# Performance work log

Hardware: AMD Instinct MI355X
Metric: run time of the kernel (lower is better)

## Reference

```python
import jax, jax.numpy as jnp
import numpy as np

HIDDEN = 100
N_NODE = 100000
B = 512
T = 50

def setup_inputs() -> dict:
    key = jax.random.key(0)
    ks = jax.random.split(key, 20)
    stdv = 1.0 / np.sqrt(HIDDEN)
    u = lambda k, shape: jax.random.uniform(k, shape, jnp.float32, -stdv, stdv)
    d = HIDDEN
    return {
        "adj_in": jax.random.uniform(ks[0], (B, T, T), jnp.float32),
        "adj_out": jax.random.uniform(ks[1], (B, T, T), jnp.float32),
        "mask": jnp.ones((B, T), jnp.float32),
        "item": jax.random.randint(ks[2], (B, T), 0, N_NODE, jnp.int32),
        "alias": jax.random.randint(ks[3], (B, T), 0, T, jnp.int32),
        "step": 1,
        "embedding": u(ks[4], (N_NODE, d)),
        "W_in": u(ks[5], (d, d)),
        "b_in": u(ks[6], (d,)),
        "W_out": u(ks[7], (d, d)),
        "b_out": u(ks[8], (d,)),
        "gru_gate_k": u(ks[9], (3 * d, 2 * d)),
        "gru_gate_b": jnp.ones((2 * d,), jnp.float32),  # TF GRUCell gate bias init = 1.0
        "gru_cand_k": u(ks[10], (3 * d, d)),
        "gru_cand_b": jnp.zeros((d,), jnp.float32),
        "nasr_w1": u(ks[11], (d, d)),
        "nasr_w2": u(ks[12], (d, d)),
        "nasr_v": u(ks[13], (1, d)),
        "nasr_b": jnp.zeros((d,), jnp.float32),
        "B_mat": u(ks[14], (2 * d, d)),
    }


def _ggnn(item, adj_in, adj_out, embedding, W_in, b_in, W_out, b_out,
          gru_gate_k, gru_gate_b, gru_cand_k, gru_cand_b, step):
    h = embedding[item]  # [B,T,d]
    d = h.shape[-1]
    for _ in range(step):
        a_in = jnp.einsum('bts,bsd->btd', adj_in, h @ W_in + b_in)
        a_out = jnp.einsum('bts,bsd->btd', adj_out, h @ W_out + b_out)
        a = jnp.concatenate([a_in, a_out], axis=-1)  # [B,T,2d]
        # TF GRUCell: gates then candidate
        gates = jax.nn.sigmoid(jnp.concatenate([a, h], -1) @ gru_gate_k + gru_gate_b)
        r, u_ = gates[..., :d], gates[..., d:]
        c = jnp.tanh(jnp.concatenate([a, r * h], -1) @ gru_cand_k + gru_cand_b)
        h = u_ * h + (1.0 - u_) * c
    return h  # [B,T,d]


def reference(adj_in, adj_out, mask, item, alias, step, embedding,
              W_in, b_in, W_out, b_out, gru_gate_k, gru_gate_b,
              gru_cand_k, gru_cand_b, nasr_w1, nasr_w2, nasr_v, nasr_b, B_mat):
    d = embedding.shape[1]
    re_emb = _ggnn(item, adj_in, adj_out, embedding, W_in, b_in, W_out, b_out,
                   gru_gate_k, gru_gate_b, gru_cand_k, gru_cand_b, step)
    rm = jnp.sum(jax.lax.stop_gradient(mask), axis=1)  # session lengths
    bidx = jnp.arange(re_emb.shape[0])
    last_id = alias[bidx, rm.astype(jnp.int32) - 1]          # [B]
    last_h = re_emb[bidx, last_id]                            # [B,d]
    seq_h = jnp.take_along_axis(re_emb, alias[..., None], axis=1)  # [B,L,d]
    last = last_h @ nasr_w1                                   # [B,d]
    seq = seq_h @ nasr_w2                                     # [B,L,d]
    m = jax.nn.sigmoid(last[:, None, :] + seq + nasr_b)       # [B,L,d]
    coef = (m @ nasr_v[0]) * mask                             # [B,L]
    ma = jnp.concatenate([jnp.sum(coef[..., None] * seq_h, axis=1), last], axis=-1)  # [B,2d]
    y1 = ma @ B_mat                                           # [B,d]
    logits = y1 @ embedding[1:].T                             # [B,n_node-1]
    return logits
```

## Files before the change

### kernel.cpp

```cpp
#include <hip/hip_runtime.h>
#include <math.h>

#define D 100
#define T 50
#define BB 512
#define NOUT 99999

__device__ __forceinline__ float sigf(float x) { return 1.f / (1.f + expf(-x)); }

__global__ __launch_bounds__(256) void ggnn_fused(
    const float* __restrict__ adj_in, const float* __restrict__ adj_out,
    const float* __restrict__ mask,   const int* __restrict__ item,
    const int* __restrict__ alias_,   const float* __restrict__ emb,
    const float* __restrict__ W_in,   const float* __restrict__ b_in,
    const float* __restrict__ W_out,  const float* __restrict__ b_out,
    const float* __restrict__ gate_k, const float* __restrict__ gate_b,
    const float* __restrict__ cand_k, const float* __restrict__ cand_b,
    const float* __restrict__ w1,     const float* __restrict__ w2,
    const float* __restrict__ v,      const float* __restrict__ nb,
    const float* __restrict__ Bm,     float* __restrict__ y1)
{
    __shared__ float hS[T*D];
    __shared__ float R1[T*D];
    __shared__ float R2[T*D];
    __shared__ float maskS[T+2], vS[D], nbS[D], lastWS[D], coefS[T+2], maS[2*D];
    __shared__ int aliasS[T+2];
    __shared__ int rmidx;

    const int b = blockIdx.x, tid = threadIdx.x;
    const size_t bT = (size_t)b * T;

    if (tid < T) {
        aliasS[tid] = alias_[bT + tid];
        maskS[tid]  = mask[bT + tid];
    }
    if (tid >= 64 && tid < 64 + D) {
        int k = tid - 64;
        vS[k] = v[k]; nbS[k] = nb[k];
    }
    for (int idx = tid; idx < T*25; idx += 256) {
        int t = idx / 25, q = idx - t*25;
        int node = item[bT + t];
        *(float4*)&hS[t*D + q*4] = *(const float4*)&emb[(size_t)node*D + q*4];
    }
    __syncthreads();
    if (tid == 0) {
        float s = 0.f;
        for (int t = 0; t < T; ++t) s += maskS[t];
        rmidx = aliasS[(int)s - 1];
    }

    const bool act250 = tid < 250;
    const int tg50  = tid / 50;
    const int rem50 = tid % 50;
    const int cg25  = tid / 25;
    const int jq25  = tid % 25;

    if (act250) {
        const int which = rem50 / 25, jq = rem50 % 25;
        const int t0 = tg50 * 10;
        const float* W  = which ? W_out : W_in;
        const float* bb = which ? b_out : b_in;
        float4 binit = *(const float4*)&bb[jq*4];
        float4 acc[10];
        #pragma unroll
        for (int tt = 0; tt < 10; ++tt) acc[tt] = binit;
        for (int k = 0; k < D; k += 2) {
            float4 wa = *(const float4*)&W[k*D + jq*4];
            float4 wb = *(const float4*)&W[(k+1)*D + jq*4];
            #pragma unroll
            for (int tt = 0; tt < 10; ++tt) {
                float2 a = *(const float2*)&hS[(t0+tt)*D + k];
                acc[tt].x += a.x*wa.x + a.y*wb.x;
                acc[tt].y += a.x*wa.y + a.y*wb.y;
                acc[tt].z += a.x*wa.z + a.y*wb.z;
                acc[tt].w += a.x*wa.w + a.y*wb.w;
            }
        }
        float* dst = which ? R2 : R1;
        #pragma unroll
        for (int tt = 0; tt < 10; ++tt)
            *(float4*)&dst[(t0+tt)*D + jq*4] = acc[tt];
    }
    __syncthreads();

    float4 eacc[10];
    if (act250) {
        const int which = rem50 / 25, jq = rem50 % 25;
        const int t0 = tg50 * 10;
        const float* adj = which ? adj_out : adj_in;
        const float* Xs  = which ? R2 : R1;
        #pragma unroll
        for (int tt = 0; tt < 10; ++tt) eacc[tt] = make_float4(0.f,0.f,0.f,0.f);
        #pragma unroll 2
        for (int s = 0; s < T; ++s) {
            float4 x = *(const float4*)&Xs[s*D + jq*4];
            const float* ap = &adj[(bT + t0)*T + s];
            #pragma unroll
            for (int tt = 0; tt < 10; ++tt) {
                float a = ap[tt*T];
                eacc[tt].x += a*x.x; eacc[tt].y += a*x.y;
                eacc[tt].z += a*x.z; eacc[tt].w += a*x.w;
            }
        }
    }
    __syncthreads();
    if (act250) {
        const int which = rem50 / 25, jq = rem50 % 25;
        const int t0 = tg50 * 10;
        float* dst = which ? R2 : R1;
        #pragma unroll
        for (int tt = 0; tt < 10; ++tt)
            *(float4*)&dst[(t0+tt)*D + jq*4] = eacc[tt];
    }
    __syncthreads();

    float4 gacc[10];
    if (act250) {
        const int nq = rem50;
        const int t0 = tg50 * 10;
        float4 ginit = *(const float4*)&gate_b[nq*4];
        #pragma unroll
        for (int tt = 0; tt < 10; ++tt) gacc[tt] = ginit;
        for (int k = 0; k < D; k += 2) {
            float4 g0a = *(const float4*)&gate_k[(size_t)k*200 + nq*4];
            float4 g0b = *(const float4*)&gate_k[(size_t)(k+1)*200 + nq*4];
            float4 g1a = *(const float4*)&gate_k[(size_t)(k+100)*200 + nq*4];
            float4 g1b = *(const float4*)&gate_k[(size_t)(k+101)*200 + nq*4];
            float4 g2a = *(const float4*)&gate_k[(size_t)(k+200)*200 + nq*4];
            float4 g2b = *(const float4*)&gate_k[(size_t)(k+201)*200 + nq*4];
            #pragma unroll
            for (int tt = 0; tt < 10; ++tt) {
                float2 a0 = *(const float2*)&R1[(t0+tt)*D + k];
                float2 a1 = *(const float2*)&R2[(t0+tt)*D + k];
                float2 a2 = *(const float2*)&hS[(t0+tt)*D + k];
                gacc[tt].x += a0.x*g0a.x + a0.y*g0b.x + a1.x*g1a.x + a1.y*g1b.x + a2.x*g2a.x + a2.y*g2b.x;
                gacc[tt].y += a0.x*g0a.y + a0.y*g0b.y + a1.x*g1a.y + a1.y*g1b.y + a2.x*g2a.y + a2.y*g2b.y;
                gacc[tt].z += a0.x*g0a.z + a0.y*g0b.z + a1.x*g1a.z + a1.y*g1b.z + a2.x*g2a.z + a2.y*g2b.z;
                gacc[tt].w += a0.x*g0a.w + a0.y*g0b.w + a1.x*g1a.w + a1.y*g1b.w + a2.x*g2a.w + a2.y*g2b.w;
            }
        }
        #pragma unroll
        for (int tt = 0; tt < 10; ++tt) {
            gacc[tt].x = sigf(gacc[tt].x); gacc[tt].y = sigf(gacc[tt].y);
            gacc[tt].z = sigf(gacc[tt].z); gacc[tt].w = sigf(gacc[tt].w);
        }
    }

    float4 cacc[5];
    if (act250) {
        const int t0 = cg25 * 5;
        float4 cinit = *(const float4*)&cand_b[jq25*4];
        #pragma unroll
        for (int tt = 0; tt < 5; ++tt) cacc[tt] = cinit;
        for (int k = 0; k < D; k += 2) {
            float4 c0a = *(const float4*)&cand_k[(size_t)k*D + jq25*4];
            float4 c0b = *(const float4*)&cand_k[(size_t)(k+1)*D + jq25*4];
            float4 c1a = *(const float4*)&cand_k[(size_t)(k+100)*D + jq25*4];
            float4 c1b = *(const float4*)&cand_k[(size_t)(k+101)*D + jq25*4];
            #pragma unroll
            for (int tt = 0; tt < 5; ++tt) {
                float2 a0 = *(const float2*)&R1[(t0+tt)*D + k];
                float2 a1 = *(const float2*)&R2[(t0+tt)*D + k];
                cacc[tt].x += a0.x*c0a.x + a0.y*c0b.x + a1.x*c1a.x + a1.y*c1b.x;
                cacc[tt].y += a0.x*c0a.y + a0.y*c0b.y + a1.x*c1a.y + a1.y*c1b.y;
                cacc[tt].z += a0.x*c0a.z + a0.y*c0b.z + a1.x*c1a.z + a1.y*c1b.z;
                cacc[tt].w += a0.x*c0a.w + a0.y*c0b.w + a1.x*c1a.w + a1.y*c1b.w;
            }
        }
    }
    __syncthreads();

    if (act250) {
        const int nq = rem50;
        const int t0 = tg50 * 10;
        if (nq < 25) {
            #pragma unroll
            for (int tt = 0; tt < 10; ++tt) {
                float4 hh = *(const float4*)&hS[(t0+tt)*D + nq*4];
                float4 g = gacc[tt];
                float4 o; o.x = g.x*hh.x; o.y = g.y*hh.y; o.z = g.z*hh.z; o.w = g.w*hh.w;
                *(float4*)&R1[(t0+tt)*D + nq*4] = o;
            }
        } else {
            #pragma unroll
            for (int tt = 0; tt < 10; ++tt)
                *(float4*)&R2[(t0+tt)*D + (nq-25)*4] = gacc[tt];
        }
    }
    __syncthreads();

    if (act250) {
        const int t0 = cg25 * 5;
        for (int k = 0; k < D; k += 2) {
            float4 c2a = *(const float4*)&cand_k[(size_t)(k+200)*D + jq25*4];
            float4 c2b = *(const float4*)&cand_k[(size_t)(k+201)*D + jq25*4];
            #pragma unroll
            for (int tt = 0; tt < 5; ++tt) {
                float2 rh = *(const float2*)&R1[(t0+tt)*D + k];
                cacc[tt].x += rh.x*c2a.x + rh.y*c2b.x;
                cacc[tt].y += rh.x*c2a.y + rh.y*c2b.y;
                cacc[tt].z += rh.x*c2a.z + rh.y*c2b.z;
                cacc[tt].w += rh.x*c2a.w + rh.y*c2b.w;
            }
        }
        #pragma unroll
        for (int tt = 0; tt < 5; ++tt) {
            float4 c4;
            c4.x = tanhf(cacc[tt].x); c4.y = tanhf(cacc[tt].y);
            c4.z = tanhf(cacc[tt].z); c4.w = tanhf(cacc[tt].w);
            float4 u4 = *(const float4*)&R2[(t0+tt)*D + jq25*4];
            float4 hh = *(const float4*)&hS[(t0+tt)*D + jq25*4];
            float4 o;
            o.x = u4.x*hh.x + (1.f-u4.x)*c4.x;
            o.y = u4.y*hh.y + (1.f-u4.y)*c4.y;
            o.z = u4.z*hh.z + (1.f-u4.z)*c4.z;
            o.w = u4.w*hh.w + (1.f-u4.w)*c4.w;
            *(float4*)&hS[(t0+tt)*D + jq25*4] = o;
        }
    }
    __syncthreads();

    if (tid < 125) {
        const int sg = tid / 25, jq = tid % 25;
        const int t0 = sg * 10;
        float4 sacc[10];
        #pragma unroll
        for (int tt = 0; tt < 10; ++tt) sacc[tt] = make_float4(0.f,0.f,0.f,0.f);
        int at[10];
        #pragma unroll
        for (int tt = 0; tt < 10; ++tt) at[tt] = aliasS[t0+tt];
        for (int k = 0; k < D; k += 2) {
            float4 wa = *(const float4*)&w2[(size_t)k*D + jq*4];
            float4 wb = *(const float4*)&w2[(size_t)(k+1)*D + jq*4];
            #pragma unroll
            for (int tt = 0; tt < 10; ++tt) {
                float2 a = *(const float2*)&hS[at[tt]*D + k];
                sacc[tt].x += a.x*wa.x + a.y*wb.x;
                sacc[tt].y += a.x*wa.y + a.y*wb.y;
                sacc[tt].z += a.x*wa.z + a.y*wb.z;
                sacc[tt].w += a.x*wa.w + a.y*wb.w;
            }
        }
        #pragma unroll
        for (int tt = 0; tt < 10; ++tt)
            *(float4*)&R1[(t0+tt)*D + jq*4] = sacc[tt];
    } else if (tid >= 128 && tid < 153) {
        const int jq = tid - 128;
        const int lid = rmidx;
        float4 acc = make_float4(0.f,0.f,0.f,0.f);
        for (int k = 0; k < D; k += 2) {
            float4 wa = *(const float4*)&w1[(size_t)k*D + jq*4];
            float4 wb = *(const float4*)&w1[(size_t)(k+1)*D + jq*4];
            float2 a = *(const float2*)&hS[lid*D + k];
            acc.x += a.x*wa.x + a.y*wb.x;
            acc.y += a.x*wa.y + a.y*wb.y;
            acc.z += a.x*wa.z + a.y*wb.z;
            acc.w += a.x*wa.w + a.y*wb.w;
        }
        *(float4*)&lastWS[jq*4] = acc;
    }
    __syncthreads();

    if (tid < T) {
        float s = 0.f;
        #pragma unroll 4
        for (int k = 0; k < D; ++k) {
            float x = lastWS[k] + R1[tid*D + k] + nbS[k];
            s += vS[k] * sigf(x);
        }
        coefS[tid] = s * maskS[tid];
    }
    __syncthreads();
    if (tid < 25) {
        float4 acc = make_float4(0.f,0.f,0.f,0.f);
        #pragma unroll 5
        for (int t = 0; t < T; ++t) {
            float c = coefS[t];
            float4 hh = *(const float4*)&hS[aliasS[t]*D + tid*4];
            acc.x += c*hh.x; acc.y += c*hh.y; acc.z += c*hh.z; acc.w += c*hh.w;
        }
        *(float4*)&maS[tid*4] = acc;
    } else if (tid >= 32 && tid < 57) {
        int j4 = tid - 32;
        *(float4*)&maS[D + j4*4] = *(const float4*)&lastWS[j4*4];
    }
    __syncthreads();
    if (tid < 25) {
        float4 acc = make_float4(0.f,0.f,0.f,0.f);
        #pragma unroll 4
        for (int k = 0; k < 2*D; ++k) {
            float a = maS[k];
            float4 w = *(const float4*)&Bm[(size_t)k*D + tid*4];
            acc.x += a*w.x; acc.y += a*w.y; acc.z += a*w.z; acc.w += a*w.w;
        }
        *(float4*)&y1[(size_t)b*D + tid*4] = acc;
    }
}

__global__ __launch_bounds__(256) void gemm_big(
    const float* __restrict__ y1,
    const float* __restrict__ emb,
    float* __restrict__ out)
{
    __shared__ float As[128*52];
    __shared__ float Bs[52*132];
    int tid = threadIdx.x;
    int tx = tid & 15, ty = tid >> 4;
    int n0 = blockIdx.x * 128;
    int m0 = blockIdx.y * 128;
    float acc[8][8] = {};

    for (int idx = tid; idx < 128*12; idx += 256) {
        int m = idx / 12, q = idx - m*12;
        *(float4*)&As[m*52 + q*4] = *(const float4*)&y1[(size_t)(m0+m)*D + q*4];
    }
    for (int idx = tid; idx < 128*12; idx += 256) {
        int n = idx / 12, q = idx - n*12;
        int gn = n0 + n;
        float4 vv = make_float4(0.f,0.f,0.f,0.f);
        if (gn < NOUT) vv = *(const float4*)&emb[(size_t)(gn+1)*D + q*4];
        Bs[(q*4+0)*132 + n] = vv.x;
        Bs[(q*4+1)*132 + n] = vv.y;
        Bs[(q*4+2)*132 + n] = vv.z;
        Bs[(q*4+3)*132 + n] = vv.w;
    }
    __syncthreads();
    float4 pfa[7], pfb[7];
    int na = 0;
    for (int idx = tid; idx < 128*13; idx += 256, ++na) {
        int m = idx / 13, q = idx - m*13;
        pfa[na] = *(const float4*)&y1[(size_t)(m0+m)*D + 48 + q*4];
    }
    int nbc = 0;
    for (int idx = tid; idx < 128*13; idx += 256, ++nbc) {
        int n = idx / 13, q = idx - n*13;
        int gn = n0 + n;
        float4 vv = make_float4(0.f,0.f,0.f,0.f);
        if (gn < NOUT) vv = *(const float4*)&emb[(size_t)(gn+1)*D + 48 + q*4];
        pfb[nbc] = vv;
    }
    #pragma unroll 4
    for (int kk = 0; kk < 48; kk += 2) {
        float2 a[8];
        #pragma unroll
        for (int i = 0; i < 8; ++i)
            a[i] = *(const float2*)&As[(ty + i*16)*52 + kk];
        float4 b00 = *(const float4*)&Bs[kk*132 + tx*4];
        float4 b01 = *(const float4*)&Bs[kk*132 + 64 + tx*4];
        float4 b10 = *(const float4*)&Bs[(kk+1)*132 + tx*4];
        float4 b11 = *(const float4*)&Bs[(kk+1)*132 + 64 + tx*4];
        #pragma unroll
        for (int i = 0; i < 8; ++i) {
            acc[i][0] += a[i].x*b00.x; acc[i][1] += a[i].x*b00.y;
            acc[i][2] += a[i].x*b00.z; acc[i][3] += a[i].x*b00.w;
            acc[i][4] += a[i].x*b01.x; acc[i][5] += a[i].x*b01.y;
            acc[i][6] += a[i].x*b01.z; acc[i][7] += a[i].x*b01.w;
            acc[i][0] += a[i].y*b10.x; acc[i][1] += a[i].y*b10.y;
            acc[i][2] += a[i].y*b10.z; acc[i][3] += a[i].y*b10.w;
            acc[i][4] += a[i].y*b11.x; acc[i][5] += a[i].y*b11.y;
            acc[i][6] += a[i].y*b11.z; acc[i][7] += a[i].y*b11.w;
        }
    }
    __syncthreads();
    na = 0;
    for (int idx = tid; idx < 128*13; idx += 256, ++na) {
        int m = idx / 13, q = idx - m*13;
        *(float4*)&As[m*52 + q*4] = pfa[na];
    }
    nbc = 0;
    for (int idx = tid; idx < 128*13; idx += 256, ++nbc) {
        int n = idx / 13, q = idx - n*13;
        float4 vv = pfb[nbc];
        Bs[(q*4+0)*132 + n] = vv.x;
        Bs[(q*4+1)*132 + n] = vv.y;
        Bs[(q*4+2)*132 + n] = vv.z;
        Bs[(q*4+3)*132 + n] = vv.w;
    }
    __syncthreads();
    #pragma unroll 4
    for (int kk = 0; kk < 52; kk += 2) {
        float2 a[8];
        #pragma unroll
        for (int i = 0; i < 8; ++i)
            a[i] = *(const float2*)&As[(ty + i*16)*52 + kk];
        float4 b00 = *(const float4*)&Bs[kk*132 + tx*4];
        float4 b01 = *(const float4*)&Bs[kk*132 + 64 + tx*4];
        float4 b10 = *(const float4*)&Bs[(kk+1)*132 + tx*4];
        float4 b11 = *(const float4*)&Bs[(kk+1)*132 + 64 + tx*4];
        #pragma unroll
        for (int i = 0; i < 8; ++i) {
            acc[i][0] += a[i].x*b00.x; acc[i][1] += a[i].x*b00.y;
            acc[i][2] += a[i].x*b00.z; acc[i][3] += a[i].x*b00.w;
            acc[i][4] += a[i].x*b01.x; acc[i][5] += a[i].x*b01.y;
            acc[i][6] += a[i].x*b01.z; acc[i][7] += a[i].x*b01.w;
            acc[i][0] += a[i].y*b10.x; acc[i][1] += a[i].y*b10.y;
            acc[i][2] += a[i].y*b10.z; acc[i][3] += a[i].y*b10.w;
            acc[i][4] += a[i].y*b11.x; acc[i][5] += a[i].y*b11.y;
            acc[i][6] += a[i].y*b11.z; acc[i][7] += a[i].y*b11.w;
        }
    }
    #pragma unroll
    for (int i = 0; i < 8; ++i) {
        int m = m0 + ty + i*16;
        #pragma unroll
        for (int half = 0; half < 2; ++half) {
            int nA = n0 + half*64 + tx*4;
            float* cp = &out[(size_t)m*NOUT + nA];
            #pragma unroll
            for (int q = 0; q < 4; ++q)
                if (nA + q < NOUT) cp[q] = acc[i][half*4+q];
        }
    }
}

extern "C" void kernel_launch(void* const* d_in, const int* in_sizes, int n_in,
                              void* d_out, int out_size, void* d_ws, size_t ws_size,
                              hipStream_t stream)
{
    const float* adj_in  = (const float*)d_in[0];
    const float* adj_out = (const float*)d_in[1];
    const float* mask    = (const float*)d_in[2];
    const int*   item    = (const int*)  d_in[3];
    const int*   alias_  = (const int*)  d_in[4];
    const float* emb     = (const float*)d_in[6];
    const float* W_in    = (const float*)d_in[7];
    const float* b_in    = (const float*)d_in[8];
    const float* W_out   = (const float*)d_in[9];
    const float* b_out   = (const float*)d_in[10];
    const float* gate_k  = (const float*)d_in[11];
    const float* gate_b  = (const float*)d_in[12];
    const float* cand_k  = (const float*)d_in[13];
    const float* cand_b  = (const float*)d_in[14];
    const float* w1      = (const float*)d_in[15];
    const float* w2      = (const float*)d_in[16];
    const float* v       = (const float*)d_in[17];
    const float* nb      = (const float*)d_in[18];
    const float* Bm      = (const float*)d_in[19];
    float* out = (float*)d_out;
    float* y1  = (float*)d_ws;

    ggnn_fused<<<BB, 256, 0, stream>>>(
        adj_in, adj_out, mask, item, alias_, emb,
        W_in, b_in, W_out, b_out, gate_k, gate_b, cand_k, cand_b,
        w1, w2, v, nb, Bm, y1);

    gemm_big<<<dim3((NOUT + 127)/128, 4), 256, 0, stream>>>(y1, emb, out);
}
```

Before: 731.1 us.

## Restructure logits GEMM to stage full embedding tile and stream y1 from global

The large output GEMM now loads the whole 128-column embedding slice (all 100 K values) into shared memory once. Each block then loops over two 128-row chunks of y1, reading A operands straight from global or cache with register double-buffering instead of staging them in LDS. Output columns are interleaved by tx so that stores coalesce across the wavefront, and the grid's y dimension is halved. This cuts repeated embedding reads and makes the output writes coalesced, at the cost of more global loads for y1 and lower parallelism per block.

```diff
diff --git a/kernel.cpp b/kernel.cpp
--- a/kernel.cpp
+++ b/kernel.cpp
@@ -298,118 +298,88 @@
     }
 }
 
+#define LDB 132
+
+#define GB_COMPUTE(Ab, kbase) do {                                            \
+    _Pragma("unroll")                                                         \
+    for (int kk = 0; kk < 4; ++kk) {                                          \
+        float bq[8];                                                          \
+        _Pragma("unroll")                                                     \
+        for (int j = 0; j < 8; ++j)                                           \
+            bq[j] = Bs[(kbase + kk)*LDB + (j>>2)*64 + (j&3)*16 + tx];         \
+        _Pragma("unroll")                                                     \
+        for (int i = 0; i < 8; ++i) {                                         \
+            float a_ = kk==0 ? Ab[i].x : kk==1 ? Ab[i].y :                    \
+                       kk==2 ? Ab[i].z : Ab[i].w;                             \
+            _Pragma("unroll")                                                 \
+            for (int j = 0; j < 8; ++j)                                       \
+                acc[i][j] += a_ * bq[j];                                      \
+        }                                                                     \
+    }                                                                         \
+} while (0)
+
 __global__ __launch_bounds__(256) void gemm_big(
     const float* __restrict__ y1,
     const float* __restrict__ emb,
     float* __restrict__ out)
 {
-    __shared__ float As[128*52];
-    __shared__ float Bs[52*132];
-    int tid = threadIdx.x;
-    int tx = tid & 15, ty = tid >> 4;
-    int n0 = blockIdx.x * 128;
-    int m0 = blockIdx.y * 128;
-    float acc[8][8] = {};
-
-    for (int idx = tid; idx < 128*12; idx += 256) {
-        int m = idx / 12, q = idx - m*12;
-        *(float4*)&As[m*52 + q*4] = *(const float4*)&y1[(size_t)(m0+m)*D + q*4];
-    }
-    for (int idx = tid; idx < 128*12; idx += 256) {
-        int n = idx / 12, q = idx - n*12;
+    __shared__ float Bs[100*LDB];
+    const int tid = threadIdx.x;
+    const int tx = tid & 15, ty = tid >> 4;
+    const int n0 = blockIdx.x * 128;
+
+    for (int idx = tid; idx < 128*25; idx += 256) {
+        int n = idx / 25, q = idx - n*25;
         int gn = n0 + n;
         float4 vv = make_float4(0.f,0.f,0.f,0.f);
         if (gn < NOUT) vv = *(const float4*)&emb[(size_t)(gn+1)*D + q*4];
-        Bs[(q*4+0)*132 + n] = vv.x;
-        Bs[(q*4+1)*132 + n] = vv.y;
-        Bs[(q*4+2)*132 + n] = vv.z;
-        Bs[(q*4+3)*132 + n] = vv.w;
-    }
-    __syncthreads();
-    float4 pfa[7], pfb[7];
-    int na = 0;
-    for (int idx = tid; idx < 128*13; idx += 256, ++na) {
-        int m = idx / 13, q = idx - m*13;
-        pfa[na] = *(const float4*)&y1[(size_t)(m0+m)*D + 48 + q*4];
-    }
-    int nbc = 0;
-    for (int idx = tid; idx < 128*13; idx += 256, ++nbc) {
-        int n = idx / 13, q = idx - n*13;
-        int gn = n0 + n;
-        float4 vv = make_float4(0.f,0.f,0.f,0.f);
-        if (gn < NOUT) vv = *(const float4*)&emb[(size_t)(gn+1)*D + 48 + q*4];
-        pfb[nbc] = vv;
-    }
-    #pragma unroll 4
-    for (int kk = 0; kk < 48; kk += 2) {
-        float2 a[8];
+        Bs[(q*4+0)*LDB + n] = vv.x;
+        Bs[(q*4+1)*LDB + n] = vv.y;
+        Bs[(q*4+2)*LDB + n] = vv.z;
+        Bs[(q*4+3)*LDB + n] = vv.w;
+    }
+    __syncthreads();
+
+    float acc[8][8];
+    float4 A0[8], A1[8];
+
+    #pragma unroll 1
+    for (int mc = 0; mc < 2; ++mc) {
+        const int m0 = blockIdx.y * 256 + mc * 128;
+
         #pragma unroll
         for (int i = 0; i < 8; ++i)
-            a[i] = *(const float2*)&As[(ty + i*16)*52 + kk];
-        float4 b00 = *(const float4*)&Bs[kk*132 + tx*4];
-        float4 b01 = *(const float4*)&Bs[kk*132 + 64 + tx*4];
-        float4 b10 = *(const float4*)&Bs[(kk+1)*132 + tx*4];
-        float4 b11 = *(const float4*)&Bs[(kk+1)*132 + 64 + tx*4];
+            #pragma unroll
+            for (int j = 0; j < 8; ++j) acc[i][j] = 0.f;
+
+        #pragma unroll
+        for (int i = 0; i < 8; ++i)
+            A0[i] = *(const float4*)&y1[(size_t)(m0 + ty + i*16)*D + 0];
+
+        int k = 0;
+        #pragma unroll 1
+        for (int it = 0; it < 12; ++it, k += 8) {
+            #pragma unroll
+            for (int i = 0; i < 8; ++i)
+                A1[i] = *(const float4*)&y1[(size_t)(m0 + ty + i*16)*D + k + 4];
+            GB_COMPUTE(A0, k);
+            #pragma unroll
+            for (int i = 0; i < 8; ++i)
+                A0[i] = *(const float4*)&y1[(size_t)(m0 + ty + i*16)*D + k + 8];
+            GB_COMPUTE(A1, k + 4);
+        }
+        GB_COMPUTE(A0, 96);
+
         #pragma unroll
         for (int i = 0; i < 8; ++i) {
-            acc[i][0] += a[i].x*b00.x; acc[i][1] += a[i].x*b00.y;
-            acc[i][2] += a[i].x*b00.z; acc[i][3] += a[i].x*b00.w;
-            acc[i][4] += a[i].x*b01.x; acc[i][5] += a[i].x*b01.y;
-            acc[i][6] += a[i].x*b01.z; acc[i][7] += a[i].x*b01.w;
-            acc[i][0] += a[i].y*b10.x; acc[i][1] += a[i].y*b10.y;
-            acc[i][2] += a[i].y*b10.z; acc[i][3] += a[i].y*b10.w;
-            acc[i][4] += a[i].y*b11.x; acc[i][5] += a[i].y*b11.y;
-            acc[i][6] += a[i].y*b11.z; acc[i][7] += a[i].y*b11.w;
-        }
-    }
-    __syncthreads();
-    na = 0;
-    for (int idx = tid; idx < 128*13; idx += 256, ++na) {
-        int m = idx / 13, q = idx - m*13;
-        *(float4*)&As[m*52 + q*4] = pfa[na];
-    }
-    nbc = 0;
-    for (int idx = tid; idx < 128*13; idx += 256, ++nbc) {
-        int n = idx / 13, q = idx - n*13;
-        float4 vv = pfb[nbc];
-        Bs[(q*4+0)*132 + n] = vv.x;
-        Bs[(q*4+1)*132 + n] = vv.y;
-        Bs[(q*4+2)*132 + n] = vv.z;
-        Bs[(q*4+3)*132 + n] = vv.w;
-    }
-    __syncthreads();
-    #pragma unroll 4
-    for (int kk = 0; kk < 52; kk += 2) {
-        float2 a[8];
-        #pragma unroll
-        for (int i = 0; i < 8; ++i)
-            a[i] = *(const float2*)&As[(ty + i*16)*52 + kk];
-        float4 b00 = *(const float4*)&Bs[kk*132 + tx*4];
-        float4 b01 = *(const float4*)&Bs[kk*132 + 64 + tx*4];
-        float4 b10 = *(const float4*)&Bs[(kk+1)*132 + tx*4];
-        float4 b11 = *(const float4*)&Bs[(kk+1)*132 + 64 + tx*4];
-        #pragma unroll
-        for (int i = 0; i < 8; ++i) {
-            acc[i][0] += a[i].x*b00.x; acc[i][1] += a[i].x*b00.y;
-            acc[i][2] += a[i].x*b00.z; acc[i][3] += a[i].x*b00.w;
-            acc[i][4] += a[i].x*b01.x; acc[i][5] += a[i].x*b01.y;
-            acc[i][6] += a[i].x*b01.z; acc[i][7] += a[i].x*b01.w;
-            acc[i][0] += a[i].y*b10.x; acc[i][1] += a[i].y*b10.y;
-            acc[i][2] += a[i].y*b10.z; acc[i][3] += a[i].y*b10.w;
-            acc[i][4] += a[i].y*b11.x; acc[i][5] += a[i].y*b11.y;
-            acc[i][6] += a[i].y*b11.z; acc[i][7] += a[i].y*b11.w;
-        }
-    }
-    #pragma unroll
-    for (int i = 0; i < 8; ++i) {
-        int m = m0 + ty + i*16;
-        #pragma unroll
-        for (int half = 0; half < 2; ++half) {
-            int nA = n0 + half*64 + tx*4;
-            float* cp = &out[(size_t)m*NOUT + nA];
-            #pragma unroll
-            for (int q = 0; q < 4; ++q)
-                if (nA + q < NOUT) cp[q] = acc[i][half*4+q];
+            size_t row = (size_t)(m0 + ty + i*16) * NOUT;
+            #pragma unroll
+            for (int h = 0; h < 2; ++h)
+                #pragma unroll
+                for (int q = 0; q < 4; ++q) {
+                    int n = n0 + h*64 + q*16 + tx;
+                    if (n < NOUT) out[row + n] = acc[i][h*4+q];
+                }
         }
     }
 }
@@ -445,5 +415,5 @@
         W_in, b_in, W_out, b_out, gate_k, gate_b, cand_k, cand_b,
         w1, w2, v, nb, Bm, y1);
 
-    gemm_big<<<dim3((NOUT + 127)/128, 4), 256, 0, stream>>>(y1, emb, out);
+    gemm_big<<<dim3((NOUT + 127)/128, 2), 256, 0, stream>>>(y1, emb, out);
 }
```

Result: faster. 646.9 us (-11.5%).
